# Kernel optimization log

Hardware: AMD Instinct MI355X
Metric: run time of the kernel (lower is better)

## Reference

```python
import jax, jax.numpy as jnp
import numpy as np

EPS = 1e-8

def setup_inputs() -> dict:
    key = jax.random.key(0)
    k1, k2, k3, k4, k5 = jax.random.split(key, 5)
    B, S, d, H = 4, 1024, 512, 8
    hd = d // H
    x = jax.random.normal(k1, (B, S, d), dtype=jnp.float32)
    V = jax.random.normal(k2, (B, S, H, hd), dtype=jnp.float32)
    # binary biological mask [B, S, S]
    M = (jax.random.uniform(k3, (B, S, S)) > 0.5).astype(jnp.float32)
    in_proj_w = jax.random.normal(k4, (3 * d, d), dtype=jnp.float32) * 0.02
    in_proj_b = jnp.zeros((3 * d,), dtype=jnp.float32)
    out_w = jax.random.normal(k5, (d, d), dtype=jnp.float32) * 0.02
    out_b = jnp.zeros((d,), dtype=jnp.float32)
    return {"x": x, "V": V, "M": M, "in_proj_w": in_proj_w,
            "in_proj_b": in_proj_b, "out_w": out_w, "out_b": out_b}


def reference(x, V, M, in_proj_w, in_proj_b, out_w, out_b):
    B, S, d = x.shape
    H, hd = V.shape[2], V.shape[3]
    # packed QKV projection (torch MHA in_proj); V slice is computed by torch
    # but its result is discarded, so only Q,K slices influence the output.
    qkv = x @ in_proj_w.T + in_proj_b            # [B, S, 3d]
    q = qkv[..., :d].reshape(B, S, H, hd).transpose(0, 2, 1, 3)        # [B,H,S,hd]
    k = qkv[..., d:2 * d].reshape(B, S, H, hd).transpose(0, 2, 1, 3)   # [B,H,S,hd]
    scores = jnp.einsum("bhqd,bhkd->bhqk", q, k) / jnp.sqrt(jnp.float32(hd))
    A = jax.nn.softmax(scores, axis=-1)           # [B,H,S,S] per-head attn weights
    # biological mask + L1 renormalization (post-hoc, as in original)
    A_sparse = A * M[:, None, :, :]
    norm = jnp.sum(jnp.abs(A_sparse), axis=-1, keepdims=True) + EPS
    A_bar = A_sparse / norm
    # custom V: [B,S,H,hd] -> [B,H,S,hd]
    Vp = V.transpose(0, 2, 1, 3)
    out = jnp.einsum("bhqk,bhkd->bhqd", A_bar, Vp)  # [B,H,S,hd]
    out = out.transpose(0, 2, 1, 3).reshape(B, S, d)
    return out @ out_w.T + out_b
```

## Files before the change

kernel.cpp:

```cpp
#include <hip/hip_runtime.h>
#include <hip/hip_bf16.h>

#define BB 4
#define SS 1024
#define DD 512
#define HH 8
#define HD 64

typedef __attribute__((ext_vector_type(8))) short bf16x8;
typedef __attribute__((ext_vector_type(4))) float f32x4;

static __device__ __forceinline__ unsigned short f2b(float f) {
  union { float f; unsigned int u; } c; c.f = f;
  return (unsigned short)((c.u + 0x7fffu + ((c.u >> 16) & 1u)) >> 16);
}

__global__ __launch_bounds__(256) void cvt_all(
    const float* __restrict__ x, const float* __restrict__ W1,
    const float* __restrict__ Wo, unsigned short* __restrict__ xb,
    unsigned short* __restrict__ W1b, unsigned short* __restrict__ Wob) {
  const int c = blockIdx.x * 256 + threadIdx.x;
  const float* src; unsigned short* dst; size_t off;
  if (c < 262144) { src = x;  dst = xb;  off = (size_t)c * 8; }
  else if (c < 327680) { src = W1; dst = W1b; off = (size_t)(c - 262144) * 8; }
  else { src = Wo; dst = Wob; off = (size_t)(c - 327680) * 8; }
  const float4 a = *(const float4*)(src + off);
  const float4 b = *(const float4*)(src + off + 4);
  union { unsigned short s[8]; uint4 v; } o;
  o.s[0] = f2b(a.x); o.s[1] = f2b(a.y); o.s[2] = f2b(a.z); o.s[3] = f2b(a.w);
  o.s[4] = f2b(b.x); o.s[5] = f2b(b.y); o.s[6] = f2b(b.z); o.s[7] = f2b(b.w);
  *(uint4*)(dst + off) = o.v;
}

__global__ __launch_bounds__(256) void vtrans(
    const float* __restrict__ V, unsigned short* __restrict__ Vt) {
  __shared__ float Ls[64][65];
  const int tid = threadIdx.x;
  const int s0 = blockIdx.x * 64, h = blockIdx.y, b = blockIdx.z;
  {
    const int r = tid >> 2, cs = (tid & 3) * 16;
    const float* src = V + ((size_t)((b * SS + s0 + r) * HH) + h) * HD + cs;
#pragma unroll
    for (int j = 0; j < 4; j++) {
      const float4 v = *(const float4*)(src + j * 4);
      Ls[r][cs + j * 4 + 0] = v.x; Ls[r][cs + j * 4 + 1] = v.y;
      Ls[r][cs + j * 4 + 2] = v.z; Ls[r][cs + j * 4 + 3] = v.w;
    }
  }
  __syncthreads();
  {
    const int d = tid >> 2, ss = (tid & 3) * 16;
    union { unsigned short s[16]; uint4 v[2]; } o;
#pragma unroll
    for (int j = 0; j < 16; j++) o.s[j] = f2b(Ls[ss + j][d]);
    unsigned short* dst =
        Vt + ((size_t)((b * HH + h) * HD + d)) * SS + s0 + ss;
    *(uint4*)dst = o.v[0];
    *(uint4*)(dst + 8) = o.v[1];
  }
}

__global__ __launch_bounds__(256) void gemm_qk(
    const unsigned short* __restrict__ xb, const unsigned short* __restrict__ W1b,
    const float* __restrict__ bias, unsigned short* __restrict__ qkb) {
  __shared__ unsigned short As[128][40];
  __shared__ unsigned short Bs[64][40];
  const int tid = threadIdx.x;
  const int lane = tid & 63, wave = tid >> 6;
  const int l16 = lane & 15, quad = lane >> 4;
  const int row0 = blockIdx.y * 128, col0 = blockIdx.x * 64;

  f32x4 acc[2][4];
#pragma unroll
  for (int i = 0; i < 2; i++)
#pragma unroll
    for (int j = 0; j < 4; j++) acc[i][j] = (f32x4){0.f, 0.f, 0.f, 0.f};

  for (int k0 = 0; k0 < DD; k0 += 32) {
    __syncthreads();
    {
      const int r = tid >> 1, cs = (tid & 1) * 16;
      const unsigned short* s = xb + (size_t)(row0 + r) * DD + k0 + cs;
      *(uint4*)&As[r][cs] = *(const uint4*)s;
      *(uint4*)&As[r][cs + 8] = *(const uint4*)(s + 8);
    }
    {
      const int r = tid >> 2, cs = (tid & 3) * 8;
      *(uint4*)&Bs[r][cs] =
          *(const uint4*)(W1b + (size_t)(col0 + r) * DD + k0 + cs);
    }
    __syncthreads();

    const bf16x8 a0 = *(const bf16x8*)&As[wave * 32 + l16][quad * 8];
    const bf16x8 a1 = *(const bf16x8*)&As[wave * 32 + 16 + l16][quad * 8];
#pragma unroll
    for (int nt = 0; nt < 4; nt++) {
      const bf16x8 bb = *(const bf16x8*)&Bs[nt * 16 + l16][quad * 8];
      acc[0][nt] = __builtin_amdgcn_mfma_f32_16x16x32_bf16(a0, bb, acc[0][nt], 0, 0, 0);
      acc[1][nt] = __builtin_amdgcn_mfma_f32_16x16x32_bf16(a1, bb, acc[1][nt], 0, 0, 0);
    }
  }

#pragma unroll
  for (int nt = 0; nt < 4; nt++) {
    const int col = col0 + nt * 16 + l16;
    const float bv = bias[col];
#pragma unroll
    for (int mi = 0; mi < 2; mi++)
#pragma unroll
      for (int reg = 0; reg < 4; reg++) {
        const int row = row0 + wave * 32 + mi * 16 + quad * 4 + reg;
        qkb[(size_t)row * 1024 + col] = f2b(acc[mi][nt][reg] + bv);
      }
  }
}

__global__ __launch_bounds__(256) void gemm_out(
    const unsigned short* __restrict__ Ab, const unsigned short* __restrict__ Wob,
    const float* __restrict__ bias, float* __restrict__ out) {
  __shared__ unsigned short As[128][40];
  __shared__ unsigned short Bs[64][40];
  const int tid = threadIdx.x;
  const int lane = tid & 63, wave = tid >> 6;
  const int l16 = lane & 15, quad = lane >> 4;
  const int row0 = blockIdx.y * 128, col0 = blockIdx.x * 64;

  f32x4 acc[2][4];
#pragma unroll
  for (int i = 0; i < 2; i++)
#pragma unroll
    for (int j = 0; j < 4; j++) acc[i][j] = (f32x4){0.f, 0.f, 0.f, 0.f};

  for (int k0 = 0; k0 < DD; k0 += 32) {
    __syncthreads();
    {
      const int r = tid >> 1, cs = (tid & 1) * 16;
      const unsigned short* s = Ab + (size_t)(row0 + r) * DD + k0 + cs;
      *(uint4*)&As[r][cs] = *(const uint4*)s;
      *(uint4*)&As[r][cs + 8] = *(const uint4*)(s + 8);
    }
    {
      const int r = tid >> 2, cs = (tid & 3) * 8;
      *(uint4*)&Bs[r][cs] =
          *(const uint4*)(Wob + (size_t)(col0 + r) * DD + k0 + cs);
    }
    __syncthreads();

    const bf16x8 a0 = *(const bf16x8*)&As[wave * 32 + l16][quad * 8];
    const bf16x8 a1 = *(const bf16x8*)&As[wave * 32 + 16 + l16][quad * 8];
#pragma unroll
    for (int nt = 0; nt < 4; nt++) {
      const bf16x8 bb = *(const bf16x8*)&Bs[nt * 16 + l16][quad * 8];
      acc[0][nt] = __builtin_amdgcn_mfma_f32_16x16x32_bf16(a0, bb, acc[0][nt], 0, 0, 0);
      acc[1][nt] = __builtin_amdgcn_mfma_f32_16x16x32_bf16(a1, bb, acc[1][nt], 0, 0, 0);
    }
  }

#pragma unroll
  for (int nt = 0; nt < 4; nt++) {
    const int col = col0 + nt * 16 + l16;
    const float bv = bias[col];
#pragma unroll
    for (int mi = 0; mi < 2; mi++)
#pragma unroll
      for (int reg = 0; reg < 4; reg++) {
        const int row = row0 + wave * 32 + mi * 16 + quad * 4 + reg;
        out[(size_t)row * DD + col] = acc[mi][nt][reg] + bv;
      }
  }
}

__global__ __launch_bounds__(256) void flash_attn_split(
    const unsigned short* __restrict__ qkb, const unsigned short* __restrict__ Vt,
    const float* __restrict__ Mmask, float* __restrict__ Opart,
    float* __restrict__ Zs, float* __restrict__ Sms) {
  __shared__ unsigned short Qs[64][72];
  __shared__ unsigned short Ks[64][72];
  __shared__ unsigned short Vs[64][72];
  __shared__ unsigned short Ps[4][16][72];

  const int tid = threadIdx.x;
  const int lane = tid & 63, wave = tid >> 6;
  const int l16 = lane & 15, quad = lane >> 4;
  const int q0 = blockIdx.x * 64;
  const int h = blockIdx.y & 7, sp = blockIdx.y >> 3;
  const int b = blockIdx.z;

  {
    const int r = tid >> 2, cs = (tid & 3) * 16;
    const unsigned short* s = qkb + (size_t)(b * SS + q0 + r) * 1024 + h * HD + cs;
    *(uint4*)&Qs[r][cs] = *(const uint4*)s;
    *(uint4*)&Qs[r][cs + 8] = *(const uint4*)(s + 8);
  }
  __syncthreads();
  const bf16x8 aQ0 = *(const bf16x8*)&Qs[wave * 16 + l16][quad * 8];
  const bf16x8 aQ1 = *(const bf16x8*)&Qs[wave * 16 + l16][32 + quad * 8];

  float Zp[4] = {0.f, 0.f, 0.f, 0.f}, Smp[4] = {0.f, 0.f, 0.f, 0.f};
  f32x4 O[4];
#pragma unroll
  for (int i = 0; i < 4; i++) O[i] = (f32x4){0.f, 0.f, 0.f, 0.f};

  const float* mbase =
      Mmask + (size_t)(b * SS + q0 + wave * 16 + quad * 4) * SS + l16;

  for (int kt = sp * 8; kt < sp * 8 + 8; kt++) {
    const int k0 = kt * 64;

    float mv[4][4];
#pragma unroll
    for (int reg = 0; reg < 4; reg++)
#pragma unroll
      for (int t = 0; t < 4; t++)
        mv[reg][t] = mbase[(size_t)reg * SS + k0 + t * 16];

    __syncthreads();
    {
      const int r = tid >> 2, cs = (tid & 3) * 16;
      const unsigned short* s =
          qkb + (size_t)(b * SS + k0 + r) * 1024 + DD + h * HD + cs;
      *(uint4*)&Ks[r][cs] = *(const uint4*)s;
      *(uint4*)&Ks[r][cs + 8] = *(const uint4*)(s + 8);
    }
    {
      const int d = tid >> 2, cs = (tid & 3) * 16;
      const unsigned short* s =
          Vt + ((size_t)((b * HH + h) * HD + d)) * SS + k0 + cs;
      *(uint4*)&Vs[d][cs] = *(const uint4*)s;
      *(uint4*)&Vs[d][cs + 8] = *(const uint4*)(s + 8);
    }
    __syncthreads();

    float Sv[4][4];
#pragma unroll
    for (int t = 0; t < 4; t++) {
      const bf16x8 bK0 = *(const bf16x8*)&Ks[t * 16 + l16][quad * 8];
      const bf16x8 bK1 = *(const bf16x8*)&Ks[t * 16 + l16][32 + quad * 8];
      f32x4 a = (f32x4){0.f, 0.f, 0.f, 0.f};
      a = __builtin_amdgcn_mfma_f32_16x16x32_bf16(aQ0, bK0, a, 0, 0, 0);
      a = __builtin_amdgcn_mfma_f32_16x16x32_bf16(aQ1, bK1, a, 0, 0, 0);
#pragma unroll
      for (int reg = 0; reg < 4; reg++) Sv[t][reg] = a[reg] * 0.125f;
    }

#pragma unroll
    for (int reg = 0; reg < 4; reg++) {
      float zl = 0.f, sl = 0.f;
#pragma unroll
      for (int t = 0; t < 4; t++) {
        const float e = __expf(Sv[t][reg]);
        zl += e;
        const float em = e * mv[reg][t];
        sl += em;
        Ps[wave][quad * 4 + reg][t * 16 + l16] = f2b(em);
      }
      Zp[reg] += zl;
      Smp[reg] += sl;
    }

    const bf16x8 aP0 = *(const bf16x8*)&Ps[wave][l16][quad * 8];
    const bf16x8 aP1 = *(const bf16x8*)&Ps[wave][l16][32 + quad * 8];
#pragma unroll
    for (int dt = 0; dt < 4; dt++) {
      const bf16x8 bV0 = *(const bf16x8*)&Vs[dt * 16 + l16][quad * 8];
      const bf16x8 bV1 = *(const bf16x8*)&Vs[dt * 16 + l16][32 + quad * 8];
      O[dt] = __builtin_amdgcn_mfma_f32_16x16x32_bf16(aP0, bV0, O[dt], 0, 0, 0);
      O[dt] = __builtin_amdgcn_mfma_f32_16x16x32_bf16(aP1, bV1, O[dt], 0, 0, 0);
    }
  }

#pragma unroll
  for (int reg = 0; reg < 4; reg++) {
    float z = Zp[reg], s = Smp[reg];
    z += __shfl_xor(z, 1); s += __shfl_xor(s, 1);
    z += __shfl_xor(z, 2); s += __shfl_xor(s, 2);
    z += __shfl_xor(z, 4); s += __shfl_xor(s, 4);
    z += __shfl_xor(z, 8); s += __shfl_xor(s, 8);
    const size_t grow =
        (size_t)(b * HH + h) * SS + q0 + wave * 16 + quad * 4 + reg;
    const size_t obase = ((size_t)sp * (BB * HH * SS) + grow) * HD;
#pragma unroll
    for (int dt = 0; dt < 4; dt++)
      Opart[obase + dt * 16 + l16] = O[dt][reg];
    if (l16 == 0) {
      Zs[(size_t)sp * (BB * HH * SS) + grow] = z;
      Sms[(size_t)sp * (BB * HH * SS) + grow] = s;
    }
  }
}

__global__ __launch_bounds__(256) void combine(
    const float* __restrict__ Opart, const float* __restrict__ Zs,
    const float* __restrict__ Sms, unsigned short* __restrict__ attnb) {
  const int idx = blockIdx.x * 256 + threadIdx.x;
  const int row = idx >> 4;
  const int d = (idx & 15) * 4;
  const int NR = BB * HH * SS;
  const float4 o0 = *(const float4*)(Opart + (size_t)row * HD + d);
  const float4 o1 = *(const float4*)(Opart + ((size_t)NR + row) * HD + d);
  const float z = Zs[row] + Zs[NR + row];
  const float s = Sms[row] + Sms[NR + row];
  const float inv = 1.0f / (s + 1e-8f * z);
  const int b = row >> 13, h = (row >> 10) & 7, q = row & 1023;
  union { unsigned short us[4]; uint2 v; } o;
  o.us[0] = f2b((o0.x + o1.x) * inv);
  o.us[1] = f2b((o0.y + o1.y) * inv);
  o.us[2] = f2b((o0.z + o1.z) * inv);
  o.us[3] = f2b((o0.w + o1.w) * inv);
  *(uint2*)(attnb + (size_t)(b * SS + q) * DD + h * HD + d) = o.v;
}

extern "C" void kernel_launch(void* const* d_in, const int* in_sizes, int n_in,
                              void* d_out, int out_size, void* d_ws,
                              size_t ws_size, hipStream_t stream) {
  const float* x = (const float*)d_in[0];
  const float* V = (const float*)d_in[1];
  const float* Mmask = (const float*)d_in[2];
  const float* in_proj_w = (const float*)d_in[3];
  const float* in_proj_b = (const float*)d_in[4];
  const float* out_w = (const float*)d_in[5];
  const float* out_b = (const float*)d_in[6];
  float* out = (float*)d_out;

  unsigned char* ws = (unsigned char*)d_ws;
  unsigned short* qkb   = (unsigned short*)(ws);
  unsigned short* xb    = (unsigned short*)(ws + (8ull << 20));
  unsigned short* W1b   = (unsigned short*)(ws + (12ull << 20));
  unsigned short* Wob   = (unsigned short*)(ws + (13ull << 20));
  unsigned short* Vt    = (unsigned short*)(ws + (14ull << 20));
  unsigned short* attnb = (unsigned short*)(ws + (18ull << 20));
  float*          Opart = (float*)(ws + (22ull << 20));
  float*          Zs    = (float*)(ws + (38ull << 20));
  float*          Sms   = (float*)(ws + (38ull << 20) + (256u << 10));

  cvt_all<<<1408, 256, 0, stream>>>(x, in_proj_w, out_w, xb, W1b, Wob);
  vtrans<<<dim3(SS / 64, HH, BB), 256, 0, stream>>>(V, Vt);
  gemm_qk<<<dim3(16, 32), 256, 0, stream>>>(xb, W1b, in_proj_b, qkb);
  flash_attn_split<<<dim3(SS / 64, 2 * HH, BB), 256, 0, stream>>>(
      qkb, Vt, Mmask, Opart, Zs, Sms);
  combine<<<2048, 256, 0, stream>>>(Opart, Zs, Sms, attnb);
  gemm_out<<<dim3(8, 32), 256, 0, stream>>>(attnb, Wob, out_b, out);
}
```

Baseline: 145.4 us.

## Transpose QK^T MFMA so mask loads vectorize and drop softmax denominator

Swaps the MFMA operand order so each lane holds four consecutive key scores for one query row. The mask can then be read as a float4 per lane, and P is written as packed 64-bit stores instead of scalar shorts. Q staging shared memory is reused as the P buffer, and the unmasked softmax sum Z is dropped entirely. The epsilon term becomes a constant 1e-12 instead of 1e-8*Z, which slightly changes behaviour for rows whose mask is all zero.

```diff
diff --git a/kernel.cpp b/kernel.cpp
--- a/kernel.cpp
+++ b/kernel.cpp
@@ -173,11 +173,10 @@
 __global__ __launch_bounds__(256) void flash_attn_split(
     const unsigned short* __restrict__ qkb, const unsigned short* __restrict__ Vt,
     const float* __restrict__ Mmask, float* __restrict__ Opart,
-    float* __restrict__ Zs, float* __restrict__ Sms) {
-  __shared__ unsigned short Qs[64][72];
+    float* __restrict__ Sms) {
+  __shared__ unsigned short QP[64][72];
   __shared__ unsigned short Ks[64][72];
   __shared__ unsigned short Vs[64][72];
-  __shared__ unsigned short Ps[4][16][72];
 
   const int tid = threadIdx.x;
   const int lane = tid & 63, wave = tid >> 6;
@@ -189,30 +188,23 @@
   {
     const int r = tid >> 2, cs = (tid & 3) * 16;
     const unsigned short* s = qkb + (size_t)(b * SS + q0 + r) * 1024 + h * HD + cs;
-    *(uint4*)&Qs[r][cs] = *(const uint4*)s;
-    *(uint4*)&Qs[r][cs + 8] = *(const uint4*)(s + 8);
+    *(uint4*)&QP[r][cs] = *(const uint4*)s;
+    *(uint4*)&QP[r][cs + 8] = *(const uint4*)(s + 8);
   }
   __syncthreads();
-  const bf16x8 aQ0 = *(const bf16x8*)&Qs[wave * 16 + l16][quad * 8];
-  const bf16x8 aQ1 = *(const bf16x8*)&Qs[wave * 16 + l16][32 + quad * 8];
-
-  float Zp[4] = {0.f, 0.f, 0.f, 0.f}, Smp[4] = {0.f, 0.f, 0.f, 0.f};
+  const bf16x8 bQ0 = *(const bf16x8*)&QP[wave * 16 + l16][quad * 8];
+  const bf16x8 bQ1 = *(const bf16x8*)&QP[wave * 16 + l16][32 + quad * 8];
+  unsigned short(*Ps)[72] = (unsigned short(*)[72]) & QP[wave * 16][0];
+
+  float Smp = 0.f;
   f32x4 O[4];
 #pragma unroll
   for (int i = 0; i < 4; i++) O[i] = (f32x4){0.f, 0.f, 0.f, 0.f};
 
-  const float* mbase =
-      Mmask + (size_t)(b * SS + q0 + wave * 16 + quad * 4) * SS + l16;
+  const float* mrow = Mmask + (size_t)(b * SS + q0 + wave * 16 + l16) * SS;
 
   for (int kt = sp * 8; kt < sp * 8 + 8; kt++) {
     const int k0 = kt * 64;
-
-    float mv[4][4];
-#pragma unroll
-    for (int reg = 0; reg < 4; reg++)
-#pragma unroll
-      for (int t = 0; t < 4; t++)
-        mv[reg][t] = mbase[(size_t)reg * SS + k0 + t * 16];
 
     __syncthreads();
     {
@@ -231,35 +223,27 @@
     }
     __syncthreads();
 
-    float Sv[4][4];
 #pragma unroll
     for (int t = 0; t < 4; t++) {
-      const bf16x8 bK0 = *(const bf16x8*)&Ks[t * 16 + l16][quad * 8];
-      const bf16x8 bK1 = *(const bf16x8*)&Ks[t * 16 + l16][32 + quad * 8];
+      const bf16x8 aK0 = *(const bf16x8*)&Ks[t * 16 + l16][quad * 8];
+      const bf16x8 aK1 = *(const bf16x8*)&Ks[t * 16 + l16][32 + quad * 8];
       f32x4 a = (f32x4){0.f, 0.f, 0.f, 0.f};
-      a = __builtin_amdgcn_mfma_f32_16x16x32_bf16(aQ0, bK0, a, 0, 0, 0);
-      a = __builtin_amdgcn_mfma_f32_16x16x32_bf16(aQ1, bK1, a, 0, 0, 0);
-#pragma unroll
-      for (int reg = 0; reg < 4; reg++) Sv[t][reg] = a[reg] * 0.125f;
-    }
-
-#pragma unroll
-    for (int reg = 0; reg < 4; reg++) {
-      float zl = 0.f, sl = 0.f;
-#pragma unroll
-      for (int t = 0; t < 4; t++) {
-        const float e = __expf(Sv[t][reg]);
-        zl += e;
-        const float em = e * mv[reg][t];
-        sl += em;
-        Ps[wave][quad * 4 + reg][t * 16 + l16] = f2b(em);
-      }
-      Zp[reg] += zl;
-      Smp[reg] += sl;
-    }
-
-    const bf16x8 aP0 = *(const bf16x8*)&Ps[wave][l16][quad * 8];
-    const bf16x8 aP1 = *(const bf16x8*)&Ps[wave][l16][32 + quad * 8];
+      a = __builtin_amdgcn_mfma_f32_16x16x32_bf16(aK0, bQ0, a, 0, 0, 0);
+      a = __builtin_amdgcn_mfma_f32_16x16x32_bf16(aK1, bQ1, a, 0, 0, 0);
+      const float4 m4 = *(const float4*)(mrow + k0 + t * 16 + quad * 4);
+      const float e0 = __expf(a[0] * 0.125f) * m4.x;
+      const float e1 = __expf(a[1] * 0.125f) * m4.y;
+      const float e2 = __expf(a[2] * 0.125f) * m4.z;
+      const float e3 = __expf(a[3] * 0.125f) * m4.w;
+      Smp += (e0 + e1) + (e2 + e3);
+      uint2 w;
+      w.x = (unsigned)f2b(e0) | ((unsigned)f2b(e1) << 16);
+      w.y = (unsigned)f2b(e2) | ((unsigned)f2b(e3) << 16);
+      *(uint2*)&Ps[l16][t * 16 + quad * 4] = w;
+    }
+
+    const bf16x8 aP0 = *(const bf16x8*)&Ps[l16][quad * 8];
+    const bf16x8 aP1 = *(const bf16x8*)&Ps[l16][32 + quad * 8];
 #pragma unroll
     for (int dt = 0; dt < 4; dt++) {
       const bf16x8 bV0 = *(const bf16x8*)&Vs[dt * 16 + l16][quad * 8];
@@ -269,38 +253,31 @@
     }
   }
 
+  Smp += __shfl_xor(Smp, 16);
+  Smp += __shfl_xor(Smp, 32);
+  const size_t grow0 = (size_t)(b * HH + h) * SS + q0 + wave * 16;
+  const int NR = BB * HH * SS;
+  if (lane < 16) Sms[(size_t)sp * NR + grow0 + lane] = Smp;
 #pragma unroll
   for (int reg = 0; reg < 4; reg++) {
-    float z = Zp[reg], s = Smp[reg];
-    z += __shfl_xor(z, 1); s += __shfl_xor(s, 1);
-    z += __shfl_xor(z, 2); s += __shfl_xor(s, 2);
-    z += __shfl_xor(z, 4); s += __shfl_xor(s, 4);
-    z += __shfl_xor(z, 8); s += __shfl_xor(s, 8);
-    const size_t grow =
-        (size_t)(b * HH + h) * SS + q0 + wave * 16 + quad * 4 + reg;
-    const size_t obase = ((size_t)sp * (BB * HH * SS) + grow) * HD;
+    const size_t obase = ((size_t)sp * NR + grow0 + quad * 4 + reg) * HD;
 #pragma unroll
     for (int dt = 0; dt < 4; dt++)
       Opart[obase + dt * 16 + l16] = O[dt][reg];
-    if (l16 == 0) {
-      Zs[(size_t)sp * (BB * HH * SS) + grow] = z;
-      Sms[(size_t)sp * (BB * HH * SS) + grow] = s;
-    }
   }
 }
 
 __global__ __launch_bounds__(256) void combine(
-    const float* __restrict__ Opart, const float* __restrict__ Zs,
-    const float* __restrict__ Sms, unsigned short* __restrict__ attnb) {
+    const float* __restrict__ Opart, const float* __restrict__ Sms,
+    unsigned short* __restrict__ attnb) {
   const int idx = blockIdx.x * 256 + threadIdx.x;
   const int row = idx >> 4;
   const int d = (idx & 15) * 4;
   const int NR = BB * HH * SS;
   const float4 o0 = *(const float4*)(Opart + (size_t)row * HD + d);
   const float4 o1 = *(const float4*)(Opart + ((size_t)NR + row) * HD + d);
-  const float z = Zs[row] + Zs[NR + row];
   const float s = Sms[row] + Sms[NR + row];
-  const float inv = 1.0f / (s + 1e-8f * z);
+  const float inv = 1.0f / (s + 1e-12f);
   const int b = row >> 13, h = (row >> 10) & 7, q = row & 1023;
   union { unsigned short us[4]; uint2 v; } o;
   o.us[0] = f2b((o0.x + o1.x) * inv);
@@ -330,14 +307,13 @@
   unsigned short* Vt    = (unsigned short*)(ws + (14ull << 20));
   unsigned short* attnb = (unsigned short*)(ws + (18ull << 20));
   float*          Opart = (float*)(ws + (22ull << 20));
-  float*          Zs    = (float*)(ws + (38ull << 20));
-  float*          Sms   = (float*)(ws + (38ull << 20) + (256u << 10));
+  float*          Sms   = (float*)(ws + (38ull << 20));
 
   cvt_all<<<1408, 256, 0, stream>>>(x, in_proj_w, out_w, xb, W1b, Wob);
   vtrans<<<dim3(SS / 64, HH, BB), 256, 0, stream>>>(V, Vt);
   gemm_qk<<<dim3(16, 32), 256, 0, stream>>>(xb, W1b, in_proj_b, qkb);
   flash_attn_split<<<dim3(SS / 64, 2 * HH, BB), 256, 0, stream>>>(
-      qkb, Vt, Mmask, Opart, Zs, Sms);
-  combine<<<2048, 256, 0, stream>>>(Opart, Zs, Sms, attnb);
+      qkb, Vt, Mmask, Opart, Sms);
+  combine<<<2048, 256, 0, stream>>>(Opart, Sms, attnb);
   gemm_out<<<dim3(8, 32), 256, 0, stream>>>(attnb, Wob, out_b, out);
 }
```

After: 150.4 us. 3.4% more time.
